# Performance work log

Hardware: AMD Instinct MI355X
Metric: run time of the kernel (lower is better)

Reference implementation:

```python
import jax, jax.numpy as jnp
import numpy as np

D_MODEL = 1024
NUM_HEADS = 16
DEPTH = D_MODEL // NUM_HEADS
B, S = 4, 1024


def setup_inputs() -> dict:
    key = jax.random.key(0)
    ks = jax.random.split(key, 9)
    scale = 0.02
    return {
        "v": jax.random.normal(ks[0], (B, S, D_MODEL), jnp.float32),
        "k": jax.random.normal(ks[1], (B, S, D_MODEL), jnp.float32),
        "q": jax.random.normal(ks[2], (B, S, D_MODEL), jnp.float32),
        "wq_w": jax.random.normal(ks[3], (D_MODEL, D_MODEL), jnp.float32) * scale,
        "wq_b": jax.random.normal(ks[4], (D_MODEL,), jnp.float32) * scale,
        "wv_w": jax.random.normal(ks[5], (D_MODEL, D_MODEL), jnp.float32) * scale,
        "wv_b": jax.random.normal(ks[6], (D_MODEL,), jnp.float32) * scale,
        "dense_w": jax.random.normal(ks[7], (D_MODEL, D_MODEL), jnp.float32) * scale,
        "dense_b": jax.random.normal(ks[8], (D_MODEL,), jnp.float32) * scale,
    }


def _split_heads(x):
    # [B, S, D] -> [B, H, S, depth]
    b, s, _ = x.shape
    return x.reshape(b, s, NUM_HEADS, DEPTH).transpose(0, 2, 1, 3)


def reference(v, k, q, wq_w, wq_b, wv_w, wv_b, dense_w, dense_b):
    # Faithful to original torch module, including its bugs:
    #   v = wv(v); k = wv(v)  (k input and wk layer unused)
    #   output = logits @ v   (raw logits, NOT softmax weights)
    del k  # unused in original forward (overwritten)
    q_p = q @ wq_w.T + wq_b
    v_p = v @ wv_w.T + wv_b
    k_p = v_p @ wv_w.T + wv_b  # k = self.wv(v) after v already projected

    qh = _split_heads(q_p)  # [B,H,S,dh]
    kh = _split_heads(k_p)
    vh = _split_heads(v_p)

    logits = jnp.einsum("bhsd,bhtd->bhst", qh, kh) / jnp.sqrt(
        jnp.asarray(DEPTH, jnp.float32)
    )  # [B,H,S,S]
    attention_weights = jax.nn.softmax(logits, axis=-1)
    # BUG preserved: uses logits, not attention_weights
    attn_out = jnp.einsum("bhst,bhtd->bhsd", logits, vh)  # [B,H,S,dh]

    concat = attn_out.transpose(0, 2, 1, 3).reshape(B, S, D_MODEL)
    output = concat @ dense_w.T + dense_b
    # dropout is identity in eval mode
    return output, attention_weights
```

## Files before the change

### kernel.cpp

```cpp
#include <hip/hip_runtime.h>
#include <hip/hip_bf16.h>

#define DM 1024
#define BS 4
#define SS 1024
#define NH 16

typedef __attribute__((ext_vector_type(8))) short bf16x8;
typedef __attribute__((ext_vector_type(4))) float f32x4;

__device__ inline unsigned short f2bf(float x) {
    union { float f; unsigned u; } v; v.f = x;
    unsigned r = v.u + 0x7fffu + ((v.u >> 16) & 1u);
    return (unsigned short)(r >> 16);
}
__device__ inline float bf2f(unsigned short u) {
    union { unsigned u; float f; } v; v.u = ((unsigned)u) << 16;
    return v.f;
}

template<typename T> __device__ inline void store1(T* p, float v);
template<> __device__ inline void store1<float>(float* p, float v) { *p = v; }
template<> __device__ inline void store1<unsigned short>(unsigned short* p, float v) { *p = f2bf(v); }

__device__ inline void glds16(const unsigned short* g, unsigned short* l) {
    __builtin_amdgcn_global_load_lds(
        (const __attribute__((address_space(1))) unsigned int*)g,
        (__attribute__((address_space(3))) unsigned int*)l, 16, 0, 0);
}

__device__ inline void cvt4(const float* src, unsigned short* dst, long long off) {
    float4 v = reinterpret_cast<const float4*>(src)[off];
    ushort4 o;
    o.x = f2bf(v.x); o.y = f2bf(v.y); o.z = f2bf(v.z); o.w = f2bf(v.w);
    reinterpret_cast<ushort4*>(dst)[off] = o;
}

__global__ __launch_bounds__(256) void cvt4_bf16(
    const float* __restrict__ q, const float* __restrict__ v,
    const float* __restrict__ wq, const float* __restrict__ wv,
    unsigned short* __restrict__ qb, unsigned short* __restrict__ vb,
    unsigned short* __restrict__ wqb, unsigned short* __restrict__ wvb)
{
    const long long NQ = (long long)BS * SS * DM / 4;
    const long long NW = (long long)DM * DM / 4;
    const long long total = 2 * NQ + 2 * NW;
    long long i = (long long)blockIdx.x * 256 + threadIdx.x;
    const long long stride = (long long)gridDim.x * 256;
    for (; i < total; i += stride) {
        if (i < NQ)                cvt4(q, qb, i);
        else if (i < 2 * NQ)       cvt4(v, vb, i - NQ);
        else if (i < 2 * NQ + NW)  cvt4(wq, wqb, i - 2 * NQ);
        else                       cvt4(wv, wvb, i - 2 * NQ - NW);
    }
}

__global__ __launch_bounds__(256) void cvt_bf16(const float* __restrict__ in,
                                                unsigned short* __restrict__ out, int n4)
{
    int i = blockIdx.x * blockDim.x + threadIdx.x;
    const int stride = gridDim.x * blockDim.x;
    for (; i < n4; i += stride) cvt4(in, out, i);
}

template<typename TO>
__global__ __launch_bounds__(256) void gemmb_bt(
    const unsigned short* __restrict__ A, int lda, long long sAb, long long sAh,
    const unsigned short* __restrict__ B, int ldb, long long sBb, long long sBh,
    TO* __restrict__ C, int ldc, long long sCb, long long sCh,
    const float* __restrict__ bias, int K, int H, float scale)
{
    __shared__ unsigned short lA[2][128 * 32];
    __shared__ unsigned short lB[2][64 * 32];

    const int tid = threadIdx.x;
    const int wid = tid >> 6, lane = tid & 63;
    const int wr = wid >> 1, wc = wid & 1;
    const int r0 = lane & 15;
    const int kq = (lane >> 4) * 8;
    const int srow = lane >> 2;
    const int scol = (lane & 3) * 8;

    const int z = blockIdx.z, zb = z / H, zh = z % H;
    const unsigned short* Ap = A + sAb * zb + sAh * zh
        + ((long long)blockIdx.y * 128 + srow) * lda + scol;
    const unsigned short* Bp = B + sBb * zb + sBh * zh
        + ((long long)blockIdx.x * 64 + srow) * ldb + scol;
    TO* Cp = C + sCb * zb + sCh * zh
        + (long long)blockIdx.y * 128 * ldc + blockIdx.x * 64;

    f32x4 acc[4][2];
    #pragma unroll
    for (int m = 0; m < 4; ++m)
        #pragma unroll
        for (int n = 0; n < 2; ++n)
            acc[m][n] = f32x4{0.f, 0.f, 0.f, 0.f};

    glds16(Ap + (long long)(wid * 32) * lda, &lA[0][wid * 1024]);
    glds16(Ap + (long long)(wid * 32 + 16) * lda, &lA[0][wid * 1024 + 512]);
    glds16(Bp + (long long)(wid * 16) * ldb, &lB[0][wid * 512]);
    __syncthreads();

    const int NT = K / 32;
    int cur = 0;
    for (int t = 0; t < NT; ++t) {
        if (t + 1 < NT) {
            glds16(Ap + (long long)(wid * 32) * lda + (t + 1) * 32, &lA[cur ^ 1][wid * 1024]);
            glds16(Ap + (long long)(wid * 32 + 16) * lda + (t + 1) * 32, &lA[cur ^ 1][wid * 1024 + 512]);
            glds16(Bp + (long long)(wid * 16) * ldb + (t + 1) * 32, &lB[cur ^ 1][wid * 512]);
        }
        bf16x8 af[4], bfr[2];
        #pragma unroll
        for (int m = 0; m < 4; ++m)
            af[m] = *reinterpret_cast<const bf16x8*>(&lA[cur][(wr * 64 + m * 16 + r0) * 32 + kq]);
        #pragma unroll
        for (int n = 0; n < 2; ++n)
            bfr[n] = *reinterpret_cast<const bf16x8*>(&lB[cur][(wc * 32 + n * 16 + r0) * 32 + kq]);
        #pragma unroll
        for (int m = 0; m < 4; ++m)
            #pragma unroll
            for (int n = 0; n < 2; ++n)
                acc[m][n] = __builtin_amdgcn_mfma_f32_16x16x32_bf16(af[m], bfr[n], acc[m][n], 0, 0, 0);
        __syncthreads();
        cur ^= 1;
    }

    const int cf = lane & 15, rf = (lane >> 4) * 4;
    #pragma unroll
    for (int m = 0; m < 4; ++m) {
        #pragma unroll
        for (int n = 0; n < 2; ++n) {
            int col = wc * 32 + n * 16 + cf;
            float bv = bias ? bias[blockIdx.x * 64 + col] : 0.0f;
            #pragma unroll
            for (int j = 0; j < 4; ++j) {
                int row = wr * 64 + m * 16 + rf + j;
                store1<TO>(&Cp[(long long)row * ldc + col], acc[m][n][j] * scale + bv);
            }
        }
    }
}

__global__ __launch_bounds__(256) void transpose_vh(const unsigned short* __restrict__ vp,
                                                    unsigned short* __restrict__ vT)
{
    __shared__ unsigned short tile[64][65];
    const int bh = blockIdx.y;
    const int b = bh >> 4, h = bh & 15;
    const long long t0 = (long long)blockIdx.x * 64;
    const int tid = threadIdx.x;
    #pragma unroll
    for (int kk = 0; kk < 4; ++kk) {
        int l = tid + kk * 256;
        int row = l >> 4, c4 = l & 15;
        const unsigned short* src = vp + ((long long)b * SS + t0 + row) * DM + h * 64 + c4 * 4;
        ushort4 val = *reinterpret_cast<const ushort4*>(src);
        tile[row][c4 * 4 + 0] = val.x;
        tile[row][c4 * 4 + 1] = val.y;
        tile[row][c4 * 4 + 2] = val.z;
        tile[row][c4 * 4 + 3] = val.w;
    }
    __syncthreads();
    #pragma unroll
    for (int kk = 0; kk < 4; ++kk) {
        int l = tid + kk * 256;
        int d = l >> 4, i4 = l & 15;
        ushort4 o;
        o.x = tile[i4 * 4 + 0][d];
        o.y = tile[i4 * 4 + 1][d];
        o.z = tile[i4 * 4 + 2][d];
        o.w = tile[i4 * 4 + 3][d];
        *reinterpret_cast<ushort4*>(vT + ((long long)bh * 64 + d) * SS + t0 + i4 * 4) = o;
    }
}

__global__ __launch_bounds__(512, 4) void fused_attn6(
    const unsigned short* __restrict__ qp,
    const unsigned short* __restrict__ kp,
    const unsigned short* __restrict__ vT,
    float* __restrict__ attnw,
    unsigned short* __restrict__ cc)
{
    constexpr int LSTR = 1032;
    __shared__ alignas(16) unsigned short S16[32 * LSTR];
    __shared__ float sW[8][32];
    __shared__ float rowI[32];

    const int tid = threadIdx.x;
    const int w = tid >> 6;
    const int lane = tid & 63;
    const int lg = lane >> 4;
    const int ln = lane & 15;
    const int z = blockIdx.y, b = z >> 4, h = z & 15;
    const int row0 = blockIdx.x * 32;

    const unsigned short* qbase = qp + ((long long)b * SS + row0) * DM + h * 64;
    const unsigned short* kbase = kp + (long long)b * SS * DM + h * 64;
    const unsigned short* vbase = vT + (long long)z * 64 * SS;

    bf16x8 qf[2][2];
    #pragma unroll
    for (int rh = 0; rh < 2; ++rh)
        #pragma unroll
        for (int ks = 0; ks < 2; ++ks)
            qf[rh][ks] = *reinterpret_cast<const bf16x8*>(
                qbase + (long long)(rh * 16 + ln) * DM + ks * 32 + lg * 8);

    float s4[2][4];
    #pragma unroll
    for (int rh = 0; rh < 2; ++rh)
        #pragma unroll
        for (int j = 0; j < 4; ++j) s4[rh][j] = 0.f;

    bf16x8 kf_cur[4];
    #pragma unroll
    for (int i = 0; i < 4; ++i) {
        const int ks = i >> 1, cf2 = i & 1;
        kf_cur[i] = *reinterpret_cast<const bf16x8*>(
            kbase + (long long)(w * 32 + cf2 * 16 + ln) * DM + ks * 32 + lg * 8);
    }
    for (int c = 0; c < 4; ++c) {
        bf16x8 kf_nxt[4];
        if (c < 3) {
            #pragma unroll
            for (int i = 0; i < 4; ++i) {
                const int ks = i >> 1, cf2 = i & 1;
                kf_nxt[i] = *reinterpret_cast<const bf16x8*>(
                    kbase + (long long)((c + 1) * 256 + w * 32 + cf2 * 16 + ln) * DM + ks * 32 + lg * 8);
            }
        }
        f32x4 sac[2][2];
        #pragma unroll
        for (int rh = 0; rh < 2; ++rh) {
            sac[rh][0] = f32x4{0.f, 0.f, 0.f, 0.f};
            sac[rh][1] = f32x4{0.f, 0.f, 0.f, 0.f};
        }
        #pragma unroll
        for (int ks = 0; ks < 2; ++ks)
            #pragma unroll
            for (int cf2 = 0; cf2 < 2; ++cf2)
                #pragma unroll
                for (int rh = 0; rh < 2; ++rh)
                    sac[rh][cf2] = __builtin_amdgcn_mfma_f32_16x16x32_bf16(
                        qf[rh][ks], kf_cur[ks * 2 + cf2], sac[rh][cf2], 0, 0, 0);

        const int colbase = c * 256 + w * 32;
        #pragma unroll
        for (int rh = 0; rh < 2; ++rh) {
            #pragma unroll
            for (int cf2 = 0; cf2 < 2; ++cf2)
                #pragma unroll
                for (int j = 0; j < 4; ++j) {
                    unsigned short ub = f2bf(sac[rh][cf2][j] * 0.125f);
                    S16[(rh * 16 + lg * 4 + j) * LSTR + colbase + cf2 * 16 + ln] = ub;
                    sac[rh][cf2][j] = bf2f(ub);
                }
            #pragma unroll
            for (int j = 0; j < 4; ++j)
                s4[rh][j] += __expf(sac[rh][0][j]) + __expf(sac[rh][1][j]);
        }
        if (c < 3) {
            #pragma unroll
            for (int i = 0; i < 4; ++i) kf_cur[i] = kf_nxt[i];
        }
    }

    #pragma unroll
    for (int rh = 0; rh < 2; ++rh)
        #pragma unroll
        for (int j = 0; j < 4; ++j) {
            #pragma unroll
            for (int o = 1; o < 16; o <<= 1)
                s4[rh][j] += __shfl_xor(s4[rh][j], o);
        }
    if (ln == 0) {
        #pragma unroll
        for (int rh = 0; rh < 2; ++rh)
            #pragma unroll
            for (int j = 0; j < 4; ++j)
                sW[w][rh * 16 + lg * 4 + j] = s4[rh][j];
    }
    __syncthreads();
    if (tid < 32) {
        float sf = 0.f;
        #pragma unroll
        for (int w2 = 0; w2 < 8; ++w2) sf += sW[w2][tid];
        rowI[tid] = 1.0f / sf;
    }
    __syncthreads();

    {
        const int rr = tid >> 8;
        const int tcol = tid & 255;
        #pragma unroll 4
        for (int it = 0; it < 16; ++it) {
            const int row = it * 2 + rr;
            float inv = rowI[row];
            uint2 sv = *reinterpret_cast<const uint2*>(&S16[row * LSTR + tcol * 4]);
            f32x4 o;
            o[0] = __expf(bf2f((unsigned short)(sv.x & 0xffffu))) * inv;
            o[1] = __expf(bf2f((unsigned short)(sv.x >> 16))) * inv;
            o[2] = __expf(bf2f((unsigned short)(sv.y & 0xffffu))) * inv;
            o[3] = __expf(bf2f((unsigned short)(sv.y >> 16))) * inv;
            __builtin_nontemporal_store(
                o, reinterpret_cast<f32x4*>(attnw + ((long long)z * SS + row0 + row) * SS + tcol * 4));
        }
    }

    {
        const int rh = w >> 2, ds = w & 3;
        f32x4 pvn = f32x4{0.f, 0.f, 0.f, 0.f};
        const unsigned short* vrow = vbase + (long long)(ds * 16 + ln) * SS;
        for (int kk = 0; kk < 32; ++kk) {
            bf16x8 sa = *reinterpret_cast<const bf16x8*>(&S16[(rh * 16 + ln) * LSTR + kk * 32 + lg * 8]);
            bf16x8 vf = *reinterpret_cast<const bf16x8*>(vrow + kk * 32 + lg * 8);
            pvn = __builtin_amdgcn_mfma_f32_16x16x32_bf16(sa, vf, pvn, 0, 0, 0);
        }
        #pragma unroll
        for (int j = 0; j < 4; ++j)
            cc[((long long)b * SS + row0 + rh * 16 + lg * 4 + j) * DM + h * 64 + ds * 16 + ln] = f2bf(pvn[j]);
    }
}

extern "C" void kernel_launch(void* const* d_in, const int* in_sizes, int n_in,
                              void* d_out, int out_size, void* d_ws, size_t ws_size,
                              hipStream_t stream) {
    (void)in_sizes; (void)n_in; (void)out_size; (void)ws_size;
    const float* v    = (const float*)d_in[0];
    const float* q    = (const float*)d_in[2];
    const float* wq_w = (const float*)d_in[3];
    const float* wq_b = (const float*)d_in[4];
    const float* wv_w = (const float*)d_in[5];
    const float* wv_b = (const float*)d_in[6];
    const float* dw   = (const float*)d_in[7];
    const float* db   = (const float*)d_in[8];

    unsigned short* q_p = (unsigned short*)d_ws;
    unsigned short* v_p = q_p + (4 << 20);
    unsigned short* k_p = v_p + (4 << 20);
    unsigned short* vT  = k_p + (4 << 20);
    unsigned short* cc  = vT  + (4 << 20);

    float* out0   = (float*)d_out;
    float* attnw  = out0 + (long long)BS * SS * DM;

    unsigned short* qb  = (unsigned short*)attnw;
    unsigned short* vb  = qb  + (4 << 20);
    unsigned short* wqb = vb  + (4 << 20);
    unsigned short* wvb = wqb + (1 << 20);
    unsigned short* dwb = q_p;

    dim3 blk(256);
    dim3 projGrid(DM / 64, BS * SS / 128, 1);

    cvt4_bf16<<<dim3(2048), blk, 0, stream>>>(q, v, wq_w, wv_w, qb, vb, wqb, wvb);

    gemmb_bt<unsigned short><<<projGrid, blk, 0, stream>>>(
        qb, DM, 0, 0, wqb, DM, 0, 0, q_p, DM, 0, 0, wq_b, DM, 1, 1.0f);
    gemmb_bt<unsigned short><<<projGrid, blk, 0, stream>>>(
        vb, DM, 0, 0, wvb, DM, 0, 0, v_p, DM, 0, 0, wv_b, DM, 1, 1.0f);
    gemmb_bt<unsigned short><<<projGrid, blk, 0, stream>>>(
        v_p, DM, 0, 0, wvb, DM, 0, 0, k_p, DM, 0, 0, wv_b, DM, 1, 1.0f);

    transpose_vh<<<dim3(16, 64), blk, 0, stream>>>(v_p, vT);

    fused_attn6<<<dim3(SS / 32, BS * NH), dim3(512), 0, stream>>>(q_p, k_p, vT, attnw, cc);

    cvt_bf16<<<dim3(256), blk, 0, stream>>>(dw, dwb, (DM * DM) / 4);
    gemmb_bt<float><<<projGrid, blk, 0, stream>>>(
        cc, DM, 0, 0, dwb, DM, 0, 0, out0, DM, 0, 0, db, DM, 1, 1.0f);
}
```

Baseline: 227.7 us.

## Deepen GEMM K-tile to 64, reorder PV before softmax store, hoist dense-weight cast

The bf16 GEMM now stages 64-wide K tiles in LDS and runs two MFMA sub-steps per tile, which halves the barrier and loop overhead per K element but doubles LDS use per block. The attention kernel now does the P·V MFMA before the exp/normalize store of the attention weights, so the matmul runs ahead of the large streaming write. When the workspace is big enough, the dense-weight bf16 conversion moves to the start into its own buffer, letting it sit away from the later dependency chain. The larger LDS footprint may lower GEMM occupancy, and the K-tile loop assumes K is a multiple of 64.

```diff
diff --git a/kernel.cpp b/kernel.cpp
--- a/kernel.cpp
+++ b/kernel.cpp
@@ -70,16 +70,16 @@
     TO* __restrict__ C, int ldc, long long sCb, long long sCh,
     const float* __restrict__ bias, int K, int H, float scale)
 {
-    __shared__ unsigned short lA[2][128 * 32];
-    __shared__ unsigned short lB[2][64 * 32];
+    __shared__ unsigned short lA[2][128 * 64];
+    __shared__ unsigned short lB[2][64 * 64];
 
     const int tid = threadIdx.x;
     const int wid = tid >> 6, lane = tid & 63;
     const int wr = wid >> 1, wc = wid & 1;
     const int r0 = lane & 15;
     const int kq = (lane >> 4) * 8;
-    const int srow = lane >> 2;
-    const int scol = (lane & 3) * 8;
+    const int srow = lane >> 3;
+    const int scol = (lane & 7) * 8;
 
     const int z = blockIdx.z, zb = z / H, zh = z % H;
     const unsigned short* Ap = A + sAb * zb + sAh * zh
@@ -96,31 +96,44 @@
         for (int n = 0; n < 2; ++n)
             acc[m][n] = f32x4{0.f, 0.f, 0.f, 0.f};
 
-    glds16(Ap + (long long)(wid * 32) * lda, &lA[0][wid * 1024]);
-    glds16(Ap + (long long)(wid * 32 + 16) * lda, &lA[0][wid * 1024 + 512]);
-    glds16(Bp + (long long)(wid * 16) * ldb, &lB[0][wid * 512]);
+    #pragma unroll
+    for (int k = 0; k < 4; ++k)
+        glds16(Ap + (long long)(wid * 32 + k * 8) * lda, &lA[0][(wid * 32 + k * 8) * 64]);
+    #pragma unroll
+    for (int k = 0; k < 2; ++k)
+        glds16(Bp + (long long)(wid * 16 + k * 8) * ldb, &lB[0][(wid * 16 + k * 8) * 64]);
     __syncthreads();
 
-    const int NT = K / 32;
+    const int NT = K / 64;
     int cur = 0;
     for (int t = 0; t < NT; ++t) {
         if (t + 1 < NT) {
-            glds16(Ap + (long long)(wid * 32) * lda + (t + 1) * 32, &lA[cur ^ 1][wid * 1024]);
-            glds16(Ap + (long long)(wid * 32 + 16) * lda + (t + 1) * 32, &lA[cur ^ 1][wid * 1024 + 512]);
-            glds16(Bp + (long long)(wid * 16) * ldb + (t + 1) * 32, &lB[cur ^ 1][wid * 512]);
-        }
-        bf16x8 af[4], bfr[2];
-        #pragma unroll
-        for (int m = 0; m < 4; ++m)
-            af[m] = *reinterpret_cast<const bf16x8*>(&lA[cur][(wr * 64 + m * 16 + r0) * 32 + kq]);
-        #pragma unroll
-        for (int n = 0; n < 2; ++n)
-            bfr[n] = *reinterpret_cast<const bf16x8*>(&lB[cur][(wc * 32 + n * 16 + r0) * 32 + kq]);
-        #pragma unroll
-        for (int m = 0; m < 4; ++m)
+            #pragma unroll
+            for (int k = 0; k < 4; ++k)
+                glds16(Ap + (long long)(wid * 32 + k * 8) * lda + (t + 1) * 64,
+                       &lA[cur ^ 1][(wid * 32 + k * 8) * 64]);
+            #pragma unroll
+            for (int k = 0; k < 2; ++k)
+                glds16(Bp + (long long)(wid * 16 + k * 8) * ldb + (t + 1) * 64,
+                       &lB[cur ^ 1][(wid * 16 + k * 8) * 64]);
+        }
+        #pragma unroll
+        for (int ks = 0; ks < 2; ++ks) {
+            bf16x8 af[4], bfr[2];
+            #pragma unroll
+            for (int m = 0; m < 4; ++m)
+                af[m] = *reinterpret_cast<const bf16x8*>(
+                    &lA[cur][(wr * 64 + m * 16 + r0) * 64 + ks * 32 + kq]);
             #pragma unroll
             for (int n = 0; n < 2; ++n)
-                acc[m][n] = __builtin_amdgcn_mfma_f32_16x16x32_bf16(af[m], bfr[n], acc[m][n], 0, 0, 0);
+                bfr[n] = *reinterpret_cast<const bf16x8*>(
+                    &lB[cur][(wc * 32 + n * 16 + r0) * 64 + ks * 32 + kq]);
+            #pragma unroll
+            for (int m = 0; m < 4; ++m)
+                #pragma unroll
+                for (int n = 0; n < 2; ++n)
+                    acc[m][n] = __builtin_amdgcn_mfma_f32_16x16x32_bf16(af[m], bfr[n], acc[m][n], 0, 0, 0);
+        }
         __syncthreads();
         cur ^= 1;
     }
@@ -174,7 +187,7 @@
     }
 }
 
-__global__ __launch_bounds__(512, 4) void fused_attn6(
+__global__ __launch_bounds__(512, 4) void fused_attn7(
     const unsigned short* __restrict__ qp,
     const unsigned short* __restrict__ kp,
     const unsigned short* __restrict__ vT,
@@ -288,6 +301,20 @@
         rowI[tid] = 1.0f / sf;
     }
     __syncthreads();
+
+    {
+        const int rh = w >> 2, ds = w & 3;
+        f32x4 pvn = f32x4{0.f, 0.f, 0.f, 0.f};
+        const unsigned short* vrow = vbase + (long long)(ds * 16 + ln) * SS;
+        for (int kk = 0; kk < 32; ++kk) {
+            bf16x8 sa = *reinterpret_cast<const bf16x8*>(&S16[(rh * 16 + ln) * LSTR + kk * 32 + lg * 8]);
+            bf16x8 vf = *reinterpret_cast<const bf16x8*>(vrow + kk * 32 + lg * 8);
+            pvn = __builtin_amdgcn_mfma_f32_16x16x32_bf16(sa, vf, pvn, 0, 0, 0);
+        }
+        #pragma unroll
+        for (int j = 0; j < 4; ++j)
+            cc[((long long)b * SS + row0 + rh * 16 + lg * 4 + j) * DM + h * 64 + ds * 16 + ln] = f2bf(pvn[j]);
+    }
 
     {
         const int rr = tid >> 8;
@@ -306,26 +333,12 @@
                 o, reinterpret_cast<f32x4*>(attnw + ((long long)z * SS + row0 + row) * SS + tcol * 4));
         }
     }
-
-    {
-        const int rh = w >> 2, ds = w & 3;
-        f32x4 pvn = f32x4{0.f, 0.f, 0.f, 0.f};
-        const unsigned short* vrow = vbase + (long long)(ds * 16 + ln) * SS;
-        for (int kk = 0; kk < 32; ++kk) {
-            bf16x8 sa = *reinterpret_cast<const bf16x8*>(&S16[(rh * 16 + ln) * LSTR + kk * 32 + lg * 8]);
-            bf16x8 vf = *reinterpret_cast<const bf16x8*>(vrow + kk * 32 + lg * 8);
-            pvn = __builtin_amdgcn_mfma_f32_16x16x32_bf16(sa, vf, pvn, 0, 0, 0);
-        }
-        #pragma unroll
-        for (int j = 0; j < 4; ++j)
-            cc[((long long)b * SS + row0 + rh * 16 + lg * 4 + j) * DM + h * 64 + ds * 16 + ln] = f2bf(pvn[j]);
-    }
 }
 
 extern "C" void kernel_launch(void* const* d_in, const int* in_sizes, int n_in,
                               void* d_out, int out_size, void* d_ws, size_t ws_size,
                               hipStream_t stream) {
-    (void)in_sizes; (void)n_in; (void)out_size; (void)ws_size;
+    (void)in_sizes; (void)n_in; (void)out_size;
     const float* v    = (const float*)d_in[0];
     const float* q    = (const float*)d_in[2];
     const float* wq_w = (const float*)d_in[3];
@@ -348,12 +361,16 @@
     unsigned short* vb  = qb  + (4 << 20);
     unsigned short* wqb = vb  + (4 << 20);
     unsigned short* wvb = wqb + (1 << 20);
-    unsigned short* dwb = q_p;
+
+    const bool big_ws = ws_size >= (size_t)(42u << 20);
+    unsigned short* dwb = big_ws ? (cc + (4 << 20)) : q_p;
 
     dim3 blk(256);
     dim3 projGrid(DM / 64, BS * SS / 128, 1);
 
     cvt4_bf16<<<dim3(2048), blk, 0, stream>>>(q, v, wq_w, wv_w, qb, vb, wqb, wvb);
+    if (big_ws)
+        cvt_bf16<<<dim3(256), blk, 0, stream>>>(dw, dwb, (DM * DM) / 4);
 
     gemmb_bt<unsigned short><<<projGrid, blk, 0, stream>>>(
         qb, DM, 0, 0, wqb, DM, 0, 0, q_p, DM, 0, 0, wq_b, DM, 1, 1.0f);
@@ -364,9 +381,10 @@
 
     transpose_vh<<<dim3(16, 64), blk, 0, stream>>>(v_p, vT);
 
-    fused_attn6<<<dim3(SS / 32, BS * NH), dim3(512), 0, stream>>>(q_p, k_p, vT, attnw, cc);
-
-    cvt_bf16<<<dim3(256), blk, 0, stream>>>(dw, dwb, (DM * DM) / 4);
+    fused_attn7<<<dim3(SS / 32, BS * NH), dim3(512), 0, stream>>>(q_p, k_p, vT, attnw, cc);
+
+    if (!big_ws)
+        cvt_bf16<<<dim3(256), blk, 0, stream>>>(dw, dwb, (DM * DM) / 4);
     gemmb_bt<float><<<projGrid, blk, 0, stream>>>(
         cc, DM, 0, 0, dwb, DM, 0, 0, out0, DM, 0, 0, db, DM, 1, 1.0f);
 }
```

Measured after the change: 221.9 us. 1.03x faster.
